# Kernel tuning notes

Measured on AMD Instinct MI355X. Metric: run time of the kernel, lower is better.

## Reference

```python
import jax, jax.numpy as jnp
import numpy as np

B, T, N, D = 16, 64, 22, 64
K, E, DT, H = 4, 8, 5, 64
KL_WEIGHT = 0.01


def setup_inputs() -> dict:
    key = jax.random.key(0)
    ks = jax.random.split(key, 4)
    x = jax.random.normal(ks[0], (B, T, N, D), jnp.float32)
    # fixed-degree neighbor table: joint j's neighbors are (j..j+3) mod N, self first
    nb = jnp.asarray((np.arange(N)[:, None] + np.arange(K)[None, :]) % N, jnp.int32)
    Fin = DT * K * D  # 1280 flattened local window feature
    W1 = jax.random.normal(ks[1], (N, E, Fin, H), jnp.float32) / np.float32(np.sqrt(Fin))
    b1 = jnp.zeros((N, E, H), jnp.float32)
    W2 = jax.random.normal(ks[2], (N, E, H, H), jnp.float32) / np.float32(np.sqrt(H))
    b2 = jnp.zeros((N, E, H), jnp.float32)
    W3 = jax.random.normal(ks[3], (N, E, H, D), jnp.float32) / np.float32(np.sqrt(H))
    b3 = jnp.zeros((N, E, D), jnp.float32)
    return {"x": x, "nb": nb, "W1": W1, "b1": b1, "W2": W2, "b2": b2, "W3": W3, "b3": b3}


def reference(x, nb, W1, b1, W2, b2, W3, b3):
    Bx, Tx, Nx, Dx = x.shape
    dt_half = DT // 2
    # all valid centers t in range(dt_half, T - dt_half - 1), batched (no python loop over t, j)
    ts = jnp.arange(dt_half, Tx - dt_half - 1)            # [Tw]
    offs = jnp.arange(-dt_half, dt_half + 1)              # [DT]
    win = x[:, ts[:, None] + offs[None, :]]               # [B,Tw,DT,N,D]
    dx = win[:, :, :, nb, :]                              # [B,Tw,DT,N,K,D] neighbor gather
    Tw = ts.shape[0]
    f = dx.transpose(0, 1, 3, 2, 4, 5).reshape(Bx, Tw, Nx, DT * K * Dx)  # [B,Tw,N,Fin]
    # per-joint per-expert MLP, fully batched
    h = jax.nn.relu(jnp.einsum('btnf,nefh->btneh', f, W1) + b1)
    h = jax.nn.relu(jnp.einsum('btneh,nehg->btneg', h, W2) + b2)
    pred = jnp.einsum('btneh,nehd->btned', h, W3) + b3    # [B,Tw,N,E,D]
    y = x[:, ts]                                          # [B,Tw,N,D] center-frame target
    err = jnp.mean((pred - y[:, :, :, None, :]) ** 2, axis=-1)  # [B,Tw,N,E]
    min_err = jnp.min(err, axis=-1)                       # winner-take-all (monopoly)
    expert_idx_all = jnp.argmin(err, axis=-1)             # [B,Tw,N]
    p = jax.nn.softmax(-err, axis=-1)
    kl = jnp.sum(p * (jnp.log(p + 1e-9) + jnp.log(jnp.float32(E))), axis=-1)  # KL to uniform
    per_tj = jnp.mean(min_err + KL_WEIGHT * kl, axis=0)   # [Tw,N] batch-mean local losses
    # original divides by the FINAL loop indices j and t (off-by-one kept for fidelity)
    total = jnp.sum(per_tj) / jnp.float32(Nx - 1) / jnp.float32(Tx - dt_half - 2)
    expert_idx = expert_idx_all[:, -1, -1]                # last (t, j) iteration, [B]
    return total, expert_idx
```

## Files before the change

### kernel.cpp

```cpp
#include <hip/hip_runtime.h>
#include <math.h>

#define B_   16
#define T_   64
#define N_   22
#define D_   64
#define K_   4
#define E_   8
#define H_   64
#define TW   59
#define M_   (B_ * TW)
#define NE_  (N_ * E_)
#define GRID (NE_ * 8)
#define NDXT (N_ * D_)
#define XTOT (B_ * T_ * N_ * D_)
#define NF4  (XTOT / 4)

typedef __attribute__((ext_vector_type(8))) short short8;
typedef __attribute__((ext_vector_type(4))) float float4v;

#define ERRWS_BYTES  ((size_t)(M_ * N_ * E_) * 4)
#define XH_OFF       (ERRWS_BYTES)

__device__ inline unsigned rtn_bf16(float f) {
    unsigned u = __float_as_uint(f);
    return (u + 0x7fffu + ((u >> 16) & 1u)) >> 16;
}

__global__ __launch_bounds__(256) void pre_kernel(
    const float* __restrict__ x, const int* __restrict__ nb,
    const float* __restrict__ W1, const float* __restrict__ b1,
    const float* __restrict__ W2, const float* __restrict__ b2,
    const float* __restrict__ W3, const float* __restrict__ b3,
    float* __restrict__ err_ws, short* __restrict__ xh,
    float* __restrict__ out)
{
    const int g   = blockIdx.x;
    const int tid = threadIdx.x;
    __shared__ __align__(16) char smem[6656];

    if (g < 128) {
        const int b = g >> 3;
        const int e = g & 7;
        const int n = N_ - 1, t = TW - 1;
        const int ne = n * E_ + e;
        const int j = tid & 63;
        const int q = tid >> 6;

        float* fbuf = (float*)smem;
        float (*part)[64] = (float(*)[64])(smem + 5120);
        float* h1s = (float*)(smem + 6144);
        float* h2s = (float*)(smem + 6400);

        if (g == 0 && tid == 0) out[0] = 0.f;

        for (int i = tid; i < 1280; i += 256) {
            int dt = i >> 8, r = i & 255;
            int k = r >> 6, d = r & 63;
            int nk = nb[n * K_ + k];
            fbuf[i] = x[(((size_t)(b * T_ + t + dt)) * N_ + nk) * D_ + d];
        }
        __syncthreads();

        const float* W1p = W1 + (size_t)ne * 1280 * 64;
        float s = 0.f;
        #pragma unroll 8
        for (int k = q * 320; k < q * 320 + 320; ++k) s += fbuf[k] * W1p[(size_t)k * 64 + j];
        part[q][j] = s;
        __syncthreads();
        if (q == 0)
            h1s[j] = fmaxf(part[0][j] + part[1][j] + part[2][j] + part[3][j]
                           + b1[(size_t)ne * H_ + j], 0.f);
        __syncthreads();

        const float* W2p = W2 + (size_t)ne * 4096;
        s = 0.f;
        #pragma unroll
        for (int k = q * 16; k < q * 16 + 16; ++k) s += h1s[k] * W2p[k * 64 + j];
        part[q][j] = s;
        __syncthreads();
        if (q == 0)
            h2s[j] = fmaxf(part[0][j] + part[1][j] + part[2][j] + part[3][j]
                           + b2[(size_t)ne * H_ + j], 0.f);
        __syncthreads();

        const float* W3p = W3 + (size_t)ne * 4096;
        s = 0.f;
        #pragma unroll
        for (int k = q * 16; k < q * 16 + 16; ++k) s += h2s[k] * W3p[k * 64 + j];
        part[q][j] = s;
        __syncthreads();
        if (q == 0) {
            float pred = part[0][j] + part[1][j] + part[2][j] + part[3][j]
                       + b3[(size_t)ne * D_ + j];
            float y = x[(((size_t)(b * T_ + t + 2)) * N_ + n) * D_ + j];
            float d = pred - y;
            float sq = d * d;
            sq += __shfl_xor(sq, 1);
            sq += __shfl_xor(sq, 2);
            sq += __shfl_xor(sq, 4);
            sq += __shfl_xor(sq, 8);
            sq += __shfl_xor(sq, 16);
            sq += __shfl_xor(sq, 32);
            if (j == 0) {
                int m = b * TW + t;
                err_ws[((size_t)m * N_ + n) * E_ + e] = sq * (1.f / 64.f);
            }
        }
    } else {
        int base = (g - 128) * 256 + tid;
        #pragma unroll
        for (int it = 0; it < 2; ++it) {
            int i = base + it * (1280 * 256);
            if (i < NF4) {
                float4 v = *(const float4*)(x + (size_t)i * 4);
                uint2 hp;
                hp.x = rtn_bf16(v.x) | (rtn_bf16(v.y) << 16);
                hp.y = rtn_bf16(v.z) | (rtn_bf16(v.w) << 16);
                *(uint2*)(xh + (size_t)i * 4) = hp;
            }
        }
    }
}

__global__ __launch_bounds__(256, 4) void moe_err_kernel(
    const float* __restrict__ x, const short* __restrict__ xh,
    const int* __restrict__ nb,
    const float* __restrict__ W1, const float* __restrict__ W2,
    const float* __restrict__ W3,
    const float* __restrict__ b1, const float* __restrict__ b2,
    const float* __restrict__ b3, float* __restrict__ err_ws)
{
    const int tid = threadIdx.x;
    const int w   = tid >> 6;
    const int L   = tid & 63;
    const int g   = blockIdx.x;
    const int e   = g & 7;
    const int mt  = (g >> 3) & 7;
    const int n   = g >> 6;
    const int ne  = n * E_ + e;

    __shared__ __align__(16) char smem[26624];
    char*  wbuf = smem;
    short* himg = (short*)(smem + 8192);

    const int lrow = L & 15;
    const int dseg = (L >> 4) * 8;
    const int ccol = L & 15;
    const int qrow = (L >> 4) * 4;
    const int rowbase = mt * 128 + w * 32;

    const short* xhrow[2];
    #pragma unroll
    for (int rt = 0; rt < 2; ++rt) {
        int m  = rowbase + rt * 16 + lrow;
        int mc = m < M_ ? m : M_ - 1;
        int b = mc / TW, t = mc % TW;
        xhrow[rt] = xh + (size_t)(b * T_ + t) * NDXT;
    }

    const int o0 = __builtin_amdgcn_readfirstlane(nb[n * K_ + 0]) * D_;
    const int o1 = __builtin_amdgcn_readfirstlane(nb[n * K_ + 1]) * D_;
    const int o2 = __builtin_amdgcn_readfirstlane(nb[n * K_ + 2]) * D_;
    const int o3 = __builtin_amdgcn_readfirstlane(nb[n * K_ + 3]) * D_;

    const float* W1ne = W1 + (size_t)ne * (1280 * 64);
    const float* W2ne = W2 + (size_t)ne * 4096;
    const float* W3ne = W3 + (size_t)ne * 4096;
    auto csrc = [&](int c) {
        return c < 20 ? (W1ne + (size_t)c * 4096) : (c == 20 ? W2ne : W3ne);
    };

    float wf[2][2][8];
    uint4 wph[2];
    auto loadWf = [&](int wb, const float* src) {
        #pragma unroll
        for (int p = 0; p < 2; ++p) {
            const int pi = 2 * w + p;
            const float* sp = src + ((pi >> 2) * 32 + (L >> 4) * 8) * 64
                                  + ((pi & 3) * 16 + (L & 15));
            #pragma unroll
            for (int j = 0; j < 8; ++j) wf[wb][p][j] = sp[j * 64];
        }
    };
    auto packW = [&](int wb) {
        #pragma unroll
        for (int p = 0; p < 2; ++p) {
            unsigned hs[8];
            #pragma unroll
            for (int j = 0; j < 8; ++j) hs[j] = rtn_bf16(wf[wb][p][j]);
            wph[p].x = hs[0] | (hs[1] << 16); wph[p].y = hs[2] | (hs[3] << 16);
            wph[p].z = hs[4] | (hs[5] << 16); wph[p].w = hs[6] | (hs[7] << 16);
        }
    };
    auto storeW = [&]() {
        #pragma unroll
        for (int p = 0; p < 2; ++p)
            *(uint4*)(wbuf + (size_t)(2 * w + p) * 1024 + (size_t)L * 16) = wph[p];
    };
    auto bfrag = [&](int s2, int cf) -> short8 {
        return *(const short8*)(wbuf + (size_t)(s2 * 4 + cf) * 1024
                                     + (size_t)L * 16);
    };

    loadWf(0, csrc(0));
    loadWf(1, csrc(1));
    packW(0);

    float4v acc1[2][4];
    #pragma unroll
    for (int rt = 0; rt < 2; ++rt)
        #pragma unroll
        for (int cf = 0; cf < 4; ++cf) acc1[rt][cf] = (float4v)0.f;

    for (int dt = 0; dt < 5; ++dt) {
        #pragma unroll
        for (int kk = 0; kk < 4; ++kk) {
            const int c = dt * 4 + kk;
            __syncthreads();
            storeW();
            __syncthreads();

            loadWf(c & 1, csrc(c + 2));

            const int okk = (kk == 0) ? o0 : ((kk == 1) ? o1 : ((kk == 2) ? o2 : o3));
            const int off = dt * NDXT + okk;

            short8 ah[2][2];
            #pragma unroll
            for (int s2 = 0; s2 < 2; ++s2)
                #pragma unroll
                for (int rt = 0; rt < 2; ++rt)
                    ah[s2][rt] = *(const short8*)(xhrow[rt] + off + s2 * 32 + dseg);

            #pragma unroll
            for (int s2 = 0; s2 < 2; ++s2)
                #pragma unroll
                for (int cf = 0; cf < 4; ++cf) {
                    short8 bh = bfrag(s2, cf);
                    #pragma unroll
                    for (int rt = 0; rt < 2; ++rt)
                        acc1[rt][cf] = __builtin_amdgcn_mfma_f32_16x16x32_bf16(ah[s2][rt], bh, acc1[rt][cf], 0, 0, 0);
                }
            packW((c + 1) & 1);
        }
    }

    __syncthreads();
    storeW();
    #pragma unroll
    for (int cf = 0; cf < 4; ++cf) {
        float bv = b1[(size_t)ne * H_ + cf * 16 + ccol];
        #pragma unroll
        for (int rt = 0; rt < 2; ++rt)
            #pragma unroll
            for (int reg = 0; reg < 4; ++reg) {
                float hv = fmaxf(acc1[rt][cf][reg] + bv, 0.f);
                himg[(w * 32 + rt * 16 + qrow + reg) * 72 + cf * 16 + ccol] =
                    (short)rtn_bf16(hv);
            }
    }
    __syncthreads();

    float4v acc2[2][4];
    #pragma unroll
    for (int rt = 0; rt < 2; ++rt)
        #pragma unroll
        for (int cf = 0; cf < 4; ++cf) acc2[rt][cf] = (float4v)0.f;
    #pragma unroll
    for (int s2 = 0; s2 < 2; ++s2) {
        short8 ha[2];
        #pragma unroll
        for (int rt = 0; rt < 2; ++rt)
            ha[rt] = *(const short8*)&himg[(w * 32 + rt * 16 + lrow) * 72 + s2 * 32 + dseg];
        #pragma unroll
        for (int cf = 0; cf < 4; ++cf) {
            short8 bh = bfrag(s2, cf);
            #pragma unroll
            for (int rt = 0; rt < 2; ++rt)
                acc2[rt][cf] = __builtin_amdgcn_mfma_f32_16x16x32_bf16(ha[rt], bh, acc2[rt][cf], 0, 0, 0);
        }
    }
    packW(1);

    __syncthreads();
    storeW();
    #pragma unroll
    for (int cf = 0; cf < 4; ++cf) {
        float bv = b2[(size_t)ne * H_ + cf * 16 + ccol];
        #pragma unroll
        for (int rt = 0; rt < 2; ++rt)
            #pragma unroll
            for (int reg = 0; reg < 4; ++reg) {
                float hv = fmaxf(acc2[rt][cf][reg] + bv, 0.f);
                himg[(w * 32 + rt * 16 + qrow + reg) * 72 + cf * 16 + ccol] =
                    (short)rtn_bf16(hv);
            }
    }
    __syncthreads();

    float4v acc3[2][4];
    #pragma unroll
    for (int rt = 0; rt < 2; ++rt)
        #pragma unroll
        for (int cf = 0; cf < 4; ++cf) acc3[rt][cf] = (float4v)0.f;
    #pragma unroll
    for (int s2 = 0; s2 < 2; ++s2) {
        short8 ha[2];
        #pragma unroll
        for (int rt = 0; rt < 2; ++rt)
            ha[rt] = *(const short8*)&himg[(w * 32 + rt * 16 + lrow) * 72 + s2 * 32 + dseg];
        #pragma unroll
        for (int cf = 0; cf < 4; ++cf) {
            short8 bh = bfrag(s2, cf);
            #pragma unroll
            for (int rt = 0; rt < 2; ++rt)
                acc3[rt][cf] = __builtin_amdgcn_mfma_f32_16x16x32_bf16(ha[rt], bh, acc3[rt][cf], 0, 0, 0);
        }
    }

    {
        float b3v[4];
        #pragma unroll
        for (int cf = 0; cf < 4; ++cf) b3v[cf] = b3[(size_t)ne * D_ + cf * 16 + ccol];

        #pragma unroll
        for (int rt = 0; rt < 2; ++rt) {
            #pragma unroll
            for (int reg = 0; reg < 4; ++reg) {
                const int m  = rowbase + rt * 16 + qrow + reg;
                const int mc = m < M_ ? m : M_ - 1;
                const int b = mc / TW, t = mc % TW;
                const float* yp = x + ((size_t)(b * T_ + t + 2) * N_ + n) * D_;
                float s = 0.f;
                #pragma unroll
                for (int cf = 0; cf < 4; ++cf) {
                    float d = acc3[rt][cf][reg] + b3v[cf] - yp[cf * 16 + ccol];
                    s += d * d;
                }
                s += __shfl_xor(s, 1);
                s += __shfl_xor(s, 2);
                s += __shfl_xor(s, 4);
                s += __shfl_xor(s, 8);
                if (ccol == 0 && m < M_ && !(n == N_ - 1 && t == TW - 1)) {
                    err_ws[((size_t)m * N_ + n) * E_ + e] = s * (1.f / 64.f);
                }
            }
        }
    }
}

__global__ __launch_bounds__(256) void moe_reduce_kernel(
    const float* __restrict__ err_ws, float* __restrict__ out)
{
    const int tid = threadIdx.x;
    const int idx = blockIdx.x * 256 + tid;
    float v = 0.f;
    if (idx < M_ * N_) {
        const int m = idx / N_, n = idx % N_;
        const float* ep = err_ws + (size_t)idx * E_;
        float ev[E_];
        float4 e0 = *(const float4*)ep;
        float4 e1 = *(const float4*)(ep + 4);
        ev[0] = e0.x; ev[1] = e0.y; ev[2] = e0.z; ev[3] = e0.w;
        ev[4] = e1.x; ev[5] = e1.y; ev[6] = e1.z; ev[7] = e1.w;
        float mn = ev[0];
        int am = 0;
        #pragma unroll
        for (int i = 1; i < E_; ++i) {
            if (ev[i] < mn) { mn = ev[i]; am = i; }
        }
        float p[E_];
        float Z = 0.f;
        #pragma unroll
        for (int i = 0; i < E_; ++i) { p[i] = expf(mn - ev[i]); Z += p[i]; }
        const float invZ = 1.f / Z;
        float kl = 0.f;
        #pragma unroll
        for (int i = 0; i < E_; ++i) {
            float q = p[i] * invZ;
            kl += q * (logf(q + 1e-9f) + 2.0794415416798357f);
        }
        v = mn + 0.01f * kl;
        const int t = m % TW, b = m / TW;
        if (t == TW - 1 && n == N_ - 1) out[1 + b] = (float)am;
    }
    __shared__ float sd[256];
    sd[tid] = v;
    __syncthreads();
    for (int s = 128; s > 0; s >>= 1) {
        if (tid < s) sd[tid] += sd[tid + s];
        __syncthreads();
    }
    if (tid == 0) atomicAdd(out, sd[0] * (1.f / 20160.f));
}

extern "C" void kernel_launch(void* const* d_in, const int* in_sizes, int n_in,
                              void* d_out, int out_size, void* d_ws, size_t ws_size,
                              hipStream_t stream)
{
    const float* x  = (const float*)d_in[0];
    const int*   nb = (const int*)d_in[1];
    const float* W1 = (const float*)d_in[2];
    const float* b1 = (const float*)d_in[3];
    const float* W2 = (const float*)d_in[4];
    const float* b2 = (const float*)d_in[5];
    const float* W3 = (const float*)d_in[6];
    const float* b3 = (const float*)d_in[7];
    float* out    = (float*)d_out;
    float* err_ws = (float*)d_ws;
    short* xh     = (short*)((char*)d_ws + XH_OFF);

    hipLaunchKernelGGL(pre_kernel, dim3(GRID), dim3(256), 0, stream,
                       x, nb, W1, b1, W2, b2, W3, b3, err_ws, xh, out);
    hipLaunchKernelGGL(moe_err_kernel, dim3(GRID), dim3(256), 0, stream,
                       x, xh, nb, W1, W2, W3, b1, b2, b3, err_ws);
    const int nred = (M_ * N_ + 255) / 256;
    hipLaunchKernelGGL(moe_reduce_kernel, dim3(nred), dim3(256), 0, stream, err_ws, out);
}
```

Measured before the change: 204.6 us.

## Prepack weights into bf16 MFMA fragment images in the pre-kernel

Adds a pre-kernel phase that reads the fp32 W1/W2/W3 once per call, rounds them to bf16 and writes them into a workspace in the exact per-lane fragment layout the MFMA loop uses. The main kernel then loads contiguous 16-byte bf16 fragments instead of strided fp32 values that it had to convert. This removes the conversion and pack work from the hot loop and stops the 8 row-tile blocks that share an expert from each re-reading and re-converting the same fp32 weights. The cost is an extra weight image in workspace: a full fp32 read plus a bf16 write in the pre-kernel, and a larger pre-kernel grid.

```diff
diff --git a/kernel.cpp b/kernel.cpp
--- a/kernel.cpp
+++ b/kernel.cpp
@@ -15,12 +15,18 @@
 #define NDXT (N_ * D_)
 #define XTOT (B_ * T_ * N_ * D_)
 #define NF4  (XTOT / 4)
+#define NCH  22
+#define CHB  8192
 
 typedef __attribute__((ext_vector_type(8))) short short8;
 typedef __attribute__((ext_vector_type(4))) float float4v;
 
 #define ERRWS_BYTES  ((size_t)(M_ * N_ * E_) * 4)
 #define XH_OFF       (ERRWS_BYTES)
+#define XIMG_BYTES   ((size_t)XTOT * 2)
+#define WIMG_OFF     (XH_OFF + XIMG_BYTES)
+
+#define PRE_GRID (1408 + 7744)
 
 __device__ inline unsigned rtn_bf16(float f) {
     unsigned u = __float_as_uint(f);
@@ -33,7 +39,7 @@
     const float* __restrict__ W2, const float* __restrict__ b2,
     const float* __restrict__ W3, const float* __restrict__ b3,
     float* __restrict__ err_ws, short* __restrict__ xh,
-    float* __restrict__ out)
+    char* __restrict__ wimg, float* __restrict__ out)
 {
     const int g   = blockIdx.x;
     const int tid = threadIdx.x;
@@ -107,7 +113,7 @@
                 err_ws[((size_t)m * N_ + n) * E_ + e] = sq * (1.f / 64.f);
             }
         }
-    } else {
+    } else if (g < 1408) {
         int base = (g - 128) * 256 + tid;
         #pragma unroll
         for (int it = 0; it < 2; ++it) {
@@ -120,14 +126,37 @@
                 *(uint2*)(xh + (size_t)i * 4) = hp;
             }
         }
+    } else {
+        int t0  = (g - 1408) * 256 + tid;
+        int L   = t0 & 63;
+        int img = (t0 >> 6) & 7;
+        int v   = t0 >> 9;
+        int chunk = v % NCH;
+        int ne    = v / NCH;
+
+        const float* src;
+        if (chunk < 20)       src = W1 + ((size_t)ne * 1280 + (size_t)chunk * 64) * 64;
+        else if (chunk == 20) src = W2 + (size_t)ne * 4096;
+        else                  src = W3 + (size_t)ne * 4096;
+
+        const int k0  = (img >> 2) * 32 + (L >> 4) * 8;
+        const int col = (img & 3) * 16 + (L & 15);
+        const float* sp = src + (size_t)k0 * 64 + col;
+
+        unsigned hs[8];
+        #pragma unroll
+        for (int j = 0; j < 8; ++j) hs[j] = rtn_bf16(sp[(size_t)j * 64]);
+        uint4 h4;
+        h4.x = hs[0] | (hs[1] << 16); h4.y = hs[2] | (hs[3] << 16);
+        h4.z = hs[4] | (hs[5] << 16); h4.w = hs[6] | (hs[7] << 16);
+        *(uint4*)(wimg + ((size_t)(ne * NCH + chunk) * 8 + img) * 1024
+                       + (size_t)L * 16) = h4;
     }
 }
 
 __global__ __launch_bounds__(256, 4) void moe_err_kernel(
     const float* __restrict__ x, const short* __restrict__ xh,
-    const int* __restrict__ nb,
-    const float* __restrict__ W1, const float* __restrict__ W2,
-    const float* __restrict__ W3,
+    const int* __restrict__ nb, const char* __restrict__ wimg,
     const float* __restrict__ b1, const float* __restrict__ b2,
     const float* __restrict__ b3, float* __restrict__ err_ws)
 {
@@ -164,48 +193,26 @@
     const int o2 = __builtin_amdgcn_readfirstlane(nb[n * K_ + 2]) * D_;
     const int o3 = __builtin_amdgcn_readfirstlane(nb[n * K_ + 3]) * D_;
 
-    const float* W1ne = W1 + (size_t)ne * (1280 * 64);
-    const float* W2ne = W2 + (size_t)ne * 4096;
-    const float* W3ne = W3 + (size_t)ne * 4096;
-    auto csrc = [&](int c) {
-        return c < 20 ? (W1ne + (size_t)c * 4096) : (c == 20 ? W2ne : W3ne);
+    const char* wsrc = wimg + (size_t)ne * NCH * CHB;
+
+    uint4 wreg[2][2];
+    auto loadW = [&](int wb, int chunk) {
+        const uint4* wp = (const uint4*)(wsrc + (size_t)chunk * CHB);
+        #pragma unroll
+        for (int p = 0; p < 2; ++p) wreg[wb][p] = wp[(2 * w + p) * 64 + L];
     };
-
-    float wf[2][2][8];
-    uint4 wph[2];
-    auto loadWf = [&](int wb, const float* src) {
-        #pragma unroll
-        for (int p = 0; p < 2; ++p) {
-            const int pi = 2 * w + p;
-            const float* sp = src + ((pi >> 2) * 32 + (L >> 4) * 8) * 64
-                                  + ((pi & 3) * 16 + (L & 15));
-            #pragma unroll
-            for (int j = 0; j < 8; ++j) wf[wb][p][j] = sp[j * 64];
-        }
-    };
-    auto packW = [&](int wb) {
-        #pragma unroll
-        for (int p = 0; p < 2; ++p) {
-            unsigned hs[8];
-            #pragma unroll
-            for (int j = 0; j < 8; ++j) hs[j] = rtn_bf16(wf[wb][p][j]);
-            wph[p].x = hs[0] | (hs[1] << 16); wph[p].y = hs[2] | (hs[3] << 16);
-            wph[p].z = hs[4] | (hs[5] << 16); wph[p].w = hs[6] | (hs[7] << 16);
-        }
-    };
-    auto storeW = [&]() {
+    auto storeW = [&](int wb) {
         #pragma unroll
         for (int p = 0; p < 2; ++p)
-            *(uint4*)(wbuf + (size_t)(2 * w + p) * 1024 + (size_t)L * 16) = wph[p];
+            *(uint4*)(wbuf + (size_t)(2 * w + p) * 1024 + (size_t)L * 16) = wreg[wb][p];
     };
     auto bfrag = [&](int s2, int cf) -> short8 {
         return *(const short8*)(wbuf + (size_t)(s2 * 4 + cf) * 1024
                                      + (size_t)L * 16);
     };
 
-    loadWf(0, csrc(0));
-    loadWf(1, csrc(1));
-    packW(0);
+    loadW(0, 0);
+    loadW(1, 1);
 
     float4v acc1[2][4];
     #pragma unroll
@@ -218,10 +225,10 @@
         for (int kk = 0; kk < 4; ++kk) {
             const int c = dt * 4 + kk;
             __syncthreads();
-            storeW();
+            storeW(c & 1);
             __syncthreads();
 
-            loadWf(c & 1, csrc(c + 2));
+            loadW(c & 1, c + 2);
 
             const int okk = (kk == 0) ? o0 : ((kk == 1) ? o1 : ((kk == 2) ? o2 : o3));
             const int off = dt * NDXT + okk;
@@ -242,12 +249,11 @@
                     for (int rt = 0; rt < 2; ++rt)
                         acc1[rt][cf] = __builtin_amdgcn_mfma_f32_16x16x32_bf16(ah[s2][rt], bh, acc1[rt][cf], 0, 0, 0);
                 }
-            packW((c + 1) & 1);
         }
     }
 
     __syncthreads();
-    storeW();
+    storeW(0);
     #pragma unroll
     for (int cf = 0; cf < 4; ++cf) {
         float bv = b1[(size_t)ne * H_ + cf * 16 + ccol];
@@ -281,10 +287,9 @@
                 acc2[rt][cf] = __builtin_amdgcn_mfma_f32_16x16x32_bf16(ha[rt], bh, acc2[rt][cf], 0, 0, 0);
         }
     }
-    packW(1);
 
     __syncthreads();
-    storeW();
+    storeW(1);
     #pragma unroll
     for (int cf = 0; cf < 4; ++cf) {
         float bv = b2[(size_t)ne * H_ + cf * 16 + ccol];
@@ -410,11 +415,12 @@
     float* out    = (float*)d_out;
     float* err_ws = (float*)d_ws;
     short* xh     = (short*)((char*)d_ws + XH_OFF);
-
-    hipLaunchKernelGGL(pre_kernel, dim3(GRID), dim3(256), 0, stream,
-                       x, nb, W1, b1, W2, b2, W3, b3, err_ws, xh, out);
+    char*  wimg   = (char*)d_ws + WIMG_OFF;
+
+    hipLaunchKernelGGL(pre_kernel, dim3(PRE_GRID), dim3(256), 0, stream,
+                       x, nb, W1, b1, W2, b2, W3, b3, err_ws, xh, wimg, out);
     hipLaunchKernelGGL(moe_err_kernel, dim3(GRID), dim3(256), 0, stream,
-                       x, xh, nb, W1, W2, W3, b1, b2, b3, err_ws);
+                       x, xh, nb, wimg, b1, b2, b3, err_ws);
     const int nred = (M_ * N_ + 255) / 256;
     hipLaunchKernelGGL(moe_reduce_kernel, dim3(nred), dim3(256), 0, stream, err_ws, out);
 }
```

Result: slower. 258.9 us (+26.6%).
